# Optimization experiments

Measured on AMD Instinct MI355X. Metric: run time of the kernel, lower is better.

The kernel has to match this reference:

```python
import jax, jax.numpy as jnp
import numpy as np
import math

H = 8  # num_heads
# mock_theta_f Taylor coefficients: K(q) = 1 + q - 2q^2 + 3q^3
COEFFS = (1.0, 1.0, -2.0, 3.0)


def setup_inputs() -> dict:
    key = jax.random.key(0)
    ks = jax.random.split(key, 12)
    B, L, E = 2, 2048, 512
    s = 0.02
    return {
        "query": jax.random.normal(ks[0], (B, L, E), jnp.float32),
        "key_": jax.random.normal(ks[1], (B, L, E), jnp.float32),
        "value": jax.random.normal(ks[2], (B, L, E), jnp.float32),
        "Wq": jax.random.normal(ks[3], (E, E), jnp.float32) * s,
        "bq": jnp.zeros((E,), jnp.float32),
        "Wk": jax.random.normal(ks[4], (E, E), jnp.float32) * s,
        "bk": jnp.zeros((E,), jnp.float32),
        "Wv": jax.random.normal(ks[5], (E, E), jnp.float32) * s,
        "bv": jnp.zeros((E,), jnp.float32),
        "Wo": jax.random.normal(ks[6], (E, E), jnp.float32) * s,
        "bo": jnp.zeros((E,), jnp.float32),
        "log_tau": jnp.zeros((), jnp.float32),  # tau = exp(0) = 1.0
    }


def _horner(q):
    a0, a1, a2, a3 = COEFFS
    val = jnp.full_like(q, a3)
    val = q * val + a2
    val = q * val + a1
    val = q * val + a0
    return jnp.maximum(val, 0.0)


def _attn(query, key_, value, Wq, bq, Wk, bk, Wv, bv, Wo, bo, log_tau):
    B, L, E = query.shape
    S = key_.shape[1]
    Hd = E // H
    scale = math.sqrt(Hd)

    Q = (query @ Wq.T + bq).reshape(B, L, H, Hd).transpose(0, 2, 1, 3)  # (B,H,L,Hd)
    K = (key_ @ Wk.T + bk).reshape(B, S, H, Hd).transpose(0, 2, 1, 3)
    V = (value @ Wv.T + bv).reshape(B, S, H, Hd).transpose(0, 2, 1, 3)

    scores = jnp.einsum("bhld,bhsd->bhls", Q, K) / scale  # (B,H,L,S)

    tau = jnp.exp(log_tau)
    q = jax.nn.sigmoid(scores / tau)
    kv = _horner(q)

    # causal mask (is_causal=True): mask strict upper triangle
    causal = jnp.triu(jnp.ones((L, S), dtype=bool), k=1)  # (L,S)
    kv = jnp.where(causal[None, None], 0.0, kv)

    denom = jnp.sum(kv, axis=-1, keepdims=True)
    weights = kv / jnp.maximum(denom, 1e-12)

    out = jnp.einsum("bhls,bhsd->bhld", weights, V)  # (B,H,L,Hd)
    out = out.transpose(0, 2, 1, 3).reshape(B, L, E)
    return out @ Wo.T + bo


def reference(query, key_, value, Wq, bq, Wk, bk, Wv, bv, Wo, bo, log_tau):
    return _attn(query, key_, value, Wq, bq, Wk, bk, Wv, bv, Wo, bo, log_tau)
```

## Files before the change

### kernel.cpp

```cpp
#include <hip/hip_runtime.h>
#include <hip/hip_bf16.h>


typedef __attribute__((ext_vector_type(8))) __bf16 bf16x8;
typedef __attribute__((ext_vector_type(4))) __bf16 bf16x4;
typedef __attribute__((ext_vector_type(4))) float f32x4;
typedef __attribute__((ext_vector_type(4))) int i32x4;

#define NB 2
#define NL 2048
#define NE 512
#define NH 8
#define HD 64
#define NROW (NB * NL)
#define NJOB 144

__device__ __forceinline__ void gload16(const void* g, void* l) {
  __builtin_amdgcn_global_load_lds(
      (const __attribute__((address_space(1))) void*)g,
      (__attribute__((address_space(3))) void*)l, 16, 0, 0);
}

__global__ __launch_bounds__(256) void cvt_all(
    const float* __restrict__ q, const float* __restrict__ k,
    const float* __restrict__ v, const float* __restrict__ w0,
    const float* __restrict__ w1, const float* __restrict__ w2,
    const float* __restrict__ w3, __bf16* __restrict__ qo,
    __bf16* __restrict__ ko, __bf16* __restrict__ vo, __bf16* __restrict__ o0,
    __bf16* __restrict__ o1, __bf16* __restrict__ o2,
    __bf16* __restrict__ o3) {
  const int gid = blockIdx.x * 256 + threadIdx.x;
  const float* s;
  __bf16* d;
  int i;
  if (gid < 3 * (1 << 19)) {
    const int seg = gid >> 19;
    i = gid & ((1 << 19) - 1);
    s = seg == 0 ? q : (seg == 1 ? k : v);
    d = seg == 0 ? qo : (seg == 1 ? ko : vo);
  } else {
    const int wid = gid - 3 * (1 << 19);
    const int seg = wid >> 16;
    i = wid & 0xFFFF;
    s = seg == 0 ? w0 : (seg == 1 ? w1 : (seg == 2 ? w2 : w3));
    d = seg == 0 ? o0 : (seg == 1 ? o1 : (seg == 2 ? o2 : o3));
  }
  float4 x = ((const float4*)s)[i];
  bf16x4 o = {(__bf16)x.x, (__bf16)x.y, (__bf16)x.z, (__bf16)x.w};
  ((bf16x4*)d)[i] = o;
}

template <int MODE>
__device__ __forceinline__ void gemm_body(const __bf16* __restrict__ A,
                                          const __bf16* __restrict__ W,
                                          const float* __restrict__ bias,
                                          __bf16* __restrict__ outb,
                                          float* __restrict__ outf) {
  __shared__ __align__(16) __bf16 As[128 * 64];
  __shared__ __align__(16) __bf16 Ws[128 * 64];

  const int tid = threadIdx.x;
  const int lane = tid & 63, w = tid >> 6;
  const int lr = lane & 15, lg = lane >> 4;
  const int brow = blockIdx.y * 128, bcol = blockIdx.x * 128;
  const int wr = (w >> 1) * 64, wc = (w & 1) * 64;

  f32x4 zero4 = {0.f, 0.f, 0.f, 0.f};
  f32x4 acc[4][4];
#pragma unroll
  for (int i = 0; i < 4; ++i)
#pragma unroll
    for (int j = 0; j < 4; ++j) acc[i][j] = zero4;

  for (int k0 = 0; k0 < NE; k0 += 64) {
    __syncthreads();
#pragma unroll
    for (int q = 0; q < 4; ++q) {
      const int cidx = tid + q * 256;
      const int rr = cidx >> 3, cc = (cidx & 7) * 8;
      gload16(A + (size_t)(brow + rr) * NE + k0 + cc, As + cidx * 8);
      gload16(W + (size_t)(bcol + rr) * NE + k0 + cc, Ws + cidx * 8);
    }
    __syncthreads();

#pragma unroll
    for (int kk = 0; kk < 2; ++kk) {
      bf16x8 af[4], wf[4];
#pragma unroll
      for (int mi = 0; mi < 4; ++mi)
        af[mi] =
            *(const bf16x8*)(As + (wr + mi * 16 + lr) * 64 + kk * 32 + lg * 8);
#pragma unroll
      for (int ni = 0; ni < 4; ++ni)
        wf[ni] =
            *(const bf16x8*)(Ws + (wc + ni * 16 + lr) * 64 + kk * 32 + lg * 8);
#pragma unroll
      for (int mi = 0; mi < 4; ++mi)
#pragma unroll
        for (int ni = 0; ni < 4; ++ni)
          acc[mi][ni] = __builtin_amdgcn_mfma_f32_16x16x32_bf16(
              af[mi], wf[ni], acc[mi][ni], 0, 0, 0);
    }
  }

#pragma unroll
  for (int mi = 0; mi < 4; ++mi) {
#pragma unroll
    for (int ni = 0; ni < 4; ++ni) {
      const int col = bcol + wc + ni * 16 + lr;
      const float bv = bias[col];
#pragma unroll
      for (int r = 0; r < 4; ++r) {
        const int row = brow + wr + mi * 16 + lg * 4 + r;
        const float v = acc[mi][ni][r] + bv;
        if (MODE == 0) {
          const int b = row >> 11, l = row & (NL - 1);
          const int h = col >> 6, d = col & 63;
          outb[(((size_t)b * NH + h) * NL + l) * HD + d] = (__bf16)v;
        } else if (MODE == 2) {
          const int b = row >> 11, l = row & (NL - 1);
          const int h = col >> 6, d = col & 63;
          outb[(((size_t)b * NH + h) * HD + d) * NL + l] = (__bf16)v;
        } else {
          outf[(size_t)row * NE + col] = v;
        }
      }
    }
  }
}

__global__ __launch_bounds__(256) void qkv_gemm(
    const __bf16* __restrict__ A0, const __bf16* __restrict__ A1,
    const __bf16* __restrict__ A2, const __bf16* __restrict__ W0,
    const __bf16* __restrict__ W1, const __bf16* __restrict__ W2,
    const float* __restrict__ b0, const float* __restrict__ b1,
    const float* __restrict__ b2, __bf16* __restrict__ O0,
    __bf16* __restrict__ O1, __bf16* __restrict__ O2) {
  const int z = blockIdx.z;
  if (z == 2) {
    gemm_body<2>(A2, W2, b2, O2, nullptr);
  } else {
    const __bf16* A = z == 0 ? A0 : A1;
    const __bf16* W = z == 0 ? W0 : W1;
    const float* bias = z == 0 ? b0 : b1;
    __bf16* O = z == 0 ? O0 : O1;
    gemm_body<0>(A, W, bias, O, nullptr);
  }
}

__global__ __launch_bounds__(256) void out_gemm(const __bf16* __restrict__ A,
                                                const __bf16* __restrict__ W,
                                                const float* __restrict__ bias,
                                                float* __restrict__ outf) {
  gemm_body<1>(A, W, bias, nullptr, outf);
}

template <int SLOTTED>
__global__ __launch_bounds__(256) void attn_kernel(
    const __bf16* __restrict__ Qg, const __bf16* __restrict__ Kg,
    const __bf16* __restrict__ VTg, float* __restrict__ numg,
    float* __restrict__ deng, const float* __restrict__ log_tau) {
  __shared__ __align__(16) __bf16 Kt[64][72];
  __shared__ __align__(16) __bf16 Vt[64][72];

  const int j = blockIdx.x;
  int qb, c;
  if (j < 32) {
    c = 0; qb = j;
  } else if (j < 60) {
    c = 1; qb = j - 28;
  } else if (j < 84) {
    c = 2; qb = j - 52;
  } else if (j < 104) {
    c = 3; qb = j - 72;
  } else if (j < 120) {
    c = 4; qb = j - 88;
  } else if (j < 132) {
    c = 5; qb = j - 100;
  } else if (j < 140) {
    c = 6; qb = j - 108;
  } else {
    c = 7; qb = j - 112;
  }
  const int bh = blockIdx.y;
  const __bf16* Qh = Qg + (size_t)bh * NL * HD;
  const __bf16* Kh = Kg + (size_t)bh * NL * HD;
  const __bf16* Vth = VTg + (size_t)bh * HD * NL;

  const int tid = threadIdx.x;
  const int lane = tid & 63, w = tid >> 6;
  const int lr = lane & 15, lg = lane >> 4;
  const float ninv = -1.44269504f / (8.0f * __expf(log_tau[0]));

  const int q0 = qb * 64;
  const int qg = q0 + w * 16 + lr;
  bf16x8 qf[2];
  qf[0] = *(const bf16x8*)(Qh + (size_t)qg * HD + lg * 8);
  qf[1] = *(const bf16x8*)(Qh + (size_t)qg * HD + 32 + lg * 8);

  f32x4 zero4 = {0.f, 0.f, 0.f, 0.f};
  f32x4 o_acc[4];
#pragma unroll
  for (int n = 0; n < 4; ++n) o_acc[n] = zero4;
  float den_l = 0.f;

  const int t0 = c * 4;
  const int t1 = min(t0 + 4, qb + 1);

  const int kr0 = tid >> 3, kc0 = (tid & 7) * 8;

  bf16x8 kpa = *(const bf16x8*)(Kh + (size_t)(t0 * 64 + kr0) * HD + kc0);
  bf16x8 kpb = *(const bf16x8*)(Kh + (size_t)(t0 * 64 + kr0 + 32) * HD + kc0);
  bf16x8 vpa = *(const bf16x8*)(Vth + (size_t)kr0 * NL + t0 * 64 + kc0);
  bf16x8 vpb = *(const bf16x8*)(Vth + (size_t)(kr0 + 32) * NL + t0 * 64 + kc0);

  const int idxA = (((lane & 16) << 1) + lr) * 4;
  const bool hi = (lane & 32) != 0;

  for (int t = t0; t < t1; ++t) {
    const int kv0 = t * 64;
    __syncthreads();
    *(bf16x8*)&Kt[kr0][kc0] = kpa;
    *(bf16x8*)&Kt[kr0 + 32][kc0] = kpb;
    *(bf16x8*)&Vt[kr0][kc0] = vpa;
    *(bf16x8*)&Vt[kr0 + 32][kc0] = vpb;
    __syncthreads();

    if (t + 1 < t1) {
      const int kn = (t + 1) * 64;
      kpa = *(const bf16x8*)(Kh + (size_t)(kn + kr0) * HD + kc0);
      kpb = *(const bf16x8*)(Kh + (size_t)(kn + kr0 + 32) * HD + kc0);
      vpa = *(const bf16x8*)(Vth + (size_t)kr0 * NL + kn + kc0);
      vpb = *(const bf16x8*)(Vth + (size_t)(kr0 + 32) * NL + kn + kc0);
    }

    f32x4 sacc[4];
#pragma unroll
    for (int si = 0; si < 4; ++si) sacc[si] = zero4;
#pragma unroll
    for (int kk = 0; kk < 2; ++kk) {
#pragma unroll
      for (int si = 0; si < 4; ++si) {
        bf16x8 kf = *(const bf16x8*)&Kt[si * 16 + lr][kk * 32 + lg * 8];
        sacc[si] = __builtin_amdgcn_mfma_f32_16x16x32_bf16(kf, qf[kk],
                                                           sacc[si], 0, 0, 0);
      }
    }

    unsigned pk[4][2];
#pragma unroll
    for (int si = 0; si < 4; ++si) {
      const int sb = kv0 + si * 16 + lg * 4;
      unsigned kbv[4];
#pragma unroll
      for (int r = 0; r < 4; ++r) {
        const float e = __builtin_amdgcn_exp2f(sacc[si][r] * ninv);
        const float qs = __builtin_amdgcn_rcpf(1.0f + e);
        float kvv = fmaf(qs, fmaf(qs, fmaf(qs, 3.0f, -2.0f), 1.0f), 1.0f);
        if (sb + r > qg) kvv = 0.0f;
        const __bf16 kb = (__bf16)kvv;
        den_l += (float)kb;
        kbv[r] = (unsigned)__builtin_bit_cast(unsigned short, kb);
      }
      pk[si][0] = kbv[0] | (kbv[1] << 16);
      pk[si][1] = kbv[2] | (kbv[3] << 16);
    }

#pragma unroll
    for (int kk = 0; kk < 2; ++kk) {
      const int sl = kk * 2, sh = kk * 2 + 1;
      const int a0 = __builtin_amdgcn_ds_bpermute(idxA, (int)pk[sl][0]);
      const int a1 = __builtin_amdgcn_ds_bpermute(idxA, (int)pk[sl][1]);
      const int b0 = __builtin_amdgcn_ds_bpermute(idxA + 64, (int)pk[sl][0]);
      const int b1 = __builtin_amdgcn_ds_bpermute(idxA + 64, (int)pk[sl][1]);
      const int c0 = __builtin_amdgcn_ds_bpermute(idxA, (int)pk[sh][0]);
      const int c1 = __builtin_amdgcn_ds_bpermute(idxA, (int)pk[sh][1]);
      const int d0 = __builtin_amdgcn_ds_bpermute(idxA + 64, (int)pk[sh][0]);
      const int d1 = __builtin_amdgcn_ds_bpermute(idxA + 64, (int)pk[sh][1]);
      i32x4 pw = {hi ? c0 : a0, hi ? c1 : a1, hi ? d0 : b0, hi ? d1 : b1};
      bf16x8 pf = __builtin_bit_cast(bf16x8, pw);
#pragma unroll
      for (int n = 0; n < 4; ++n) {
        bf16x8 vf = *(const bf16x8*)&Vt[n * 16 + lr][kk * 32 + lg * 8];
        o_acc[n] = __builtin_amdgcn_mfma_f32_16x16x32_bf16(pf, vf, o_acc[n],
                                                           0, 0, 0);
      }
    }
  }

  den_l += __shfl_xor(den_l, 16, 64);
  den_l += __shfl_xor(den_l, 32, 64);

  if (SLOTTED) {
    float* nslot = numg + (((size_t)bh * NJOB + j) << 12);
    const int lrow = w * 16 + lg * 4;
    if (lg == 0) {
      float* dslot = deng + (((size_t)bh * NJOB + j) << 6);
      dslot[w * 16 + lr] = den_l;
    }
#pragma unroll
    for (int n = 0; n < 4; ++n) {
      const int col = n * 16 + lr;
#pragma unroll
      for (int r = 0; r < 4; ++r) nslot[(lrow + r) * 64 + col] = o_acc[n][r];
    }
  } else {
    const int orow = q0 + w * 16 + lg * 4;
    if (lg == 0) atomicAdd(&deng[(size_t)bh * NL + q0 + w * 16 + lr], den_l);
#pragma unroll
    for (int n = 0; n < 4; ++n) {
      const int col = n * 16 + lr;
#pragma unroll
      for (int r = 0; r < 4; ++r)
        atomicAdd(&numg[((size_t)bh * NL + orow + r) * HD + col], o_acc[n][r]);
    }
  }
}

__global__ __launch_bounds__(256) void combine_slotted(
    const float* __restrict__ numS, const float* __restrict__ denS,
    __bf16* __restrict__ AO) {
  const int gid = blockIdx.x * 256 + threadIdx.x;
  const int d4 = gid & 15;
  const int row = gid >> 4;
  const int bh = row >> 11, l = row & (NL - 1);
  const int b = bh >> 3, h = bh & 7;
  const int qb = l >> 6, lrow = l & 63;
  const int nc = (qb >> 2) + 1;

  f32x4 acc = {0.f, 0.f, 0.f, 0.f};
  float d = 0.f;
  for (int c = 0; c < nc; ++c) {
    const int jj = qb + 2 * c * (15 - c);
    const size_t sb = (size_t)bh * NJOB + jj;
    acc += *(const f32x4*)(numS + ((sb << 6) + lrow) * 64 + d4 * 4);
    d += denS[(sb << 6) + lrow];
  }
  const float idv = __builtin_amdgcn_rcpf(fmaxf(d, 1e-12f));
  bf16x4 o = {(__bf16)(acc[0] * idv), (__bf16)(acc[1] * idv),
              (__bf16)(acc[2] * idv), (__bf16)(acc[3] * idv)};
  *(bf16x4*)&AO[((size_t)b * NL + l) * NE + h * HD + d4 * 4] = o;
}

__global__ __launch_bounds__(256) void combine_kernel(
    const float* __restrict__ numg, const float* __restrict__ deng,
    __bf16* __restrict__ AO) {
  const int gid = blockIdx.x * 256 + threadIdx.x;
  const int d4 = gid & 15;
  const int row = gid >> 4;
  const int bh = row >> 11, l = row & (NL - 1);
  const int b = bh >> 3, h = bh & 7;
  f32x4 n4 = ((const f32x4*)numg)[gid];
  const float idv = __builtin_amdgcn_rcpf(fmaxf(deng[row], 1e-12f));
  bf16x4 o = {(__bf16)(n4[0] * idv), (__bf16)(n4[1] * idv),
              (__bf16)(n4[2] * idv), (__bf16)(n4[3] * idv)};
  *(bf16x4*)&AO[((size_t)b * NL + l) * NE + h * HD + d4 * 4] = o;
}

extern "C" void kernel_launch(void* const* d_in, const int* in_sizes, int n_in,
                              void* d_out, int out_size, void* d_ws,
                              size_t ws_size, hipStream_t stream) {
  const float* query = (const float*)d_in[0];
  const float* key_ = (const float*)d_in[1];
  const float* value = (const float*)d_in[2];
  const float* Wq = (const float*)d_in[3];
  const float* bq = (const float*)d_in[4];
  const float* Wk = (const float*)d_in[5];
  const float* bk = (const float*)d_in[6];
  const float* Wv = (const float*)d_in[7];
  const float* bv = (const float*)d_in[8];
  const float* Wo = (const float*)d_in[9];
  const float* bo = (const float*)d_in[10];
  const float* log_tau = (const float*)d_in[11];

  char* ws = (char*)d_ws;
  const size_t MB = 1024 * 1024;
  const bool slotted = (ws_size >= 55 * MB);

  __bf16* xb = (__bf16*)(ws + 0 * MB);
  __bf16* kxb = (__bf16*)(ws + 4 * MB);
  __bf16* vxb = (__bf16*)(ws + 8 * MB);

  __bf16 *wqb, *wkb, *wvb, *wob, *Qh, *Kh, *VT, *AO;
  float *numb, *denb;
  if (slotted) {
    numb = (float*)(ws + 0 * MB);
    denb = (float*)(ws + 36 * MB);
    wqb = (__bf16*)(ws + 37 * MB);
    wkb = (__bf16*)(ws + 37 * MB + 512 * 1024);
    wvb = (__bf16*)(ws + 38 * MB);
    wob = (__bf16*)(ws + 38 * MB + 512 * 1024);
    Qh = (__bf16*)(ws + 39 * MB);
    Kh = (__bf16*)(ws + 43 * MB);
    VT = (__bf16*)(ws + 47 * MB);
    AO = (__bf16*)(ws + 51 * MB);
  } else {
    numb = (float*)(ws + 0 * MB);
    denb = (float*)(ws + 8 * MB);
    wqb = (__bf16*)(ws + 12 * MB);
    wkb = (__bf16*)(ws + 12 * MB + 512 * 1024);
    wvb = (__bf16*)(ws + 13 * MB);
    wob = (__bf16*)(ws + 13 * MB + 512 * 1024);
    Qh = (__bf16*)(ws + 14 * MB);
    Kh = (__bf16*)(ws + 18 * MB);
    VT = (__bf16*)(ws + 22 * MB);
    AO = (__bf16*)(ws + 26 * MB);
  }

  cvt_all<<<7168, 256, 0, stream>>>(query, key_, value, Wq, Wk, Wv, Wo, xb,
                                    kxb, vxb, wqb, wkb, wvb, wob);

  dim3 gq(NE / 128, NROW / 128, 3);
  qkv_gemm<<<gq, 256, 0, stream>>>(xb, kxb, vxb, wqb, wkb, wvb, bq, bk, bv, Qh,
                                   Kh, VT);

  dim3 ga(NJOB, NB * NH);
  if (slotted) {
    attn_kernel<1><<<ga, 256, 0, stream>>>(Qh, Kh, VT, numb, denb, log_tau);
    combine_slotted<<<2048, 256, 0, stream>>>(numb, denb, AO);
  } else {
    hipMemsetAsync(ws, 0, 8 * MB + 128 * 1024, stream);
    attn_kernel<0><<<ga, 256, 0, stream>>>(Qh, Kh, VT, numb, denb, log_tau);
    combine_kernel<<<2048, 256, 0, stream>>>(numb, denb, AO);
  }

  dim3 gg(NE / 128, NROW / 128);
  out_gemm<<<gg, 256, 0, stream>>>(AO, wob, bo, (float*)d_out);
}
```

Measured before the change: 78.07 us.

## Fuse slotted combine into attention via last-block-arrives counter reduction

```diff
diff --git a/kernel.cpp b/kernel.cpp
--- a/kernel.cpp
+++ b/kernel.cpp
@@ -27,8 +27,12 @@
     const float* __restrict__ w1, const float* __restrict__ w2,
     const float* __restrict__ w3, __bf16* __restrict__ qo,
     __bf16* __restrict__ ko, __bf16* __restrict__ vo, __bf16* __restrict__ o0,
-    __bf16* __restrict__ o1, __bf16* __restrict__ o2,
-    __bf16* __restrict__ o3) {
+    __bf16* __restrict__ o1, __bf16* __restrict__ o2, __bf16* __restrict__ o3,
+    int* __restrict__ cnt) {
+  if (blockIdx.x == 7168) {
+    ((int2*)cnt)[threadIdx.x] = make_int2(0, 0);
+    return;
+  }
   const int gid = blockIdx.x * 256 + threadIdx.x;
   const float* s;
   __bf16* d;
@@ -159,9 +163,11 @@
 __global__ __launch_bounds__(256) void attn_kernel(
     const __bf16* __restrict__ Qg, const __bf16* __restrict__ Kg,
     const __bf16* __restrict__ VTg, float* __restrict__ numg,
-    float* __restrict__ deng, const float* __restrict__ log_tau) {
+    float* __restrict__ deng, __bf16* __restrict__ AO,
+    int* __restrict__ cnt, const float* __restrict__ log_tau) {
   __shared__ __align__(16) __bf16 Kt[64][72];
   __shared__ __align__(16) __bf16 Vt[64][72];
+  __shared__ int s_last;
 
   const int j = blockIdx.x;
   int qb, c;
@@ -293,7 +299,7 @@
 
   if (SLOTTED) {
     float* nslot = numg + (((size_t)bh * NJOB + j) << 12);
-    const int lrow = w * 16 + lg * 4;
+    const int lrow0 = w * 16 + lg * 4;
     if (lg == 0) {
       float* dslot = deng + (((size_t)bh * NJOB + j) << 6);
       dslot[w * 16 + lr] = den_l;
@@ -302,7 +308,36 @@
     for (int n = 0; n < 4; ++n) {
       const int col = n * 16 + lr;
 #pragma unroll
-      for (int r = 0; r < 4; ++r) nslot[(lrow + r) * 64 + col] = o_acc[n][r];
+      for (int r = 0; r < 4; ++r) nslot[(lrow0 + r) * 64 + col] = o_acc[n][r];
+    }
+
+    const int nc = (qb >> 2) + 1;
+    __syncthreads();
+    if (tid == 0) {
+      __threadfence();
+      const int old = atomicAdd(&cnt[bh * 32 + qb], 1);
+      s_last = (old == nc - 1) ? 1 : 0;
+    }
+    __syncthreads();
+    if (s_last) {
+      __threadfence();
+      const int b = bh >> 3, h = bh & 7;
+      for (int e = tid; e < 1024; e += 256) {
+        const int lrow = e >> 4, d4 = e & 15;
+        f32x4 acc = zero4;
+        float dsum = 0.f;
+        for (int cc2 = 0; cc2 < nc; ++cc2) {
+          const int jj = qb + 2 * cc2 * (15 - cc2);
+          const size_t sb = (size_t)bh * NJOB + jj;
+          acc += *(const f32x4*)(numg + ((sb << 6) + lrow) * 64 + d4 * 4);
+          dsum += deng[(sb << 6) + lrow];
+        }
+        const float idv = __builtin_amdgcn_rcpf(fmaxf(dsum, 1e-12f));
+        const int l = q0 + lrow;
+        bf16x4 o = {(__bf16)(acc[0] * idv), (__bf16)(acc[1] * idv),
+                    (__bf16)(acc[2] * idv), (__bf16)(acc[3] * idv)};
+        *(bf16x4*)&AO[((size_t)b * NL + l) * NE + h * HD + d4 * 4] = o;
+      }
     }
   } else {
     const int orow = q0 + w * 16 + lg * 4;
@@ -315,31 +350,6 @@
         atomicAdd(&numg[((size_t)bh * NL + orow + r) * HD + col], o_acc[n][r]);
     }
   }
-}
-
-__global__ __launch_bounds__(256) void combine_slotted(
-    const float* __restrict__ numS, const float* __restrict__ denS,
-    __bf16* __restrict__ AO) {
-  const int gid = blockIdx.x * 256 + threadIdx.x;
-  const int d4 = gid & 15;
-  const int row = gid >> 4;
-  const int bh = row >> 11, l = row & (NL - 1);
-  const int b = bh >> 3, h = bh & 7;
-  const int qb = l >> 6, lrow = l & 63;
-  const int nc = (qb >> 2) + 1;
-
-  f32x4 acc = {0.f, 0.f, 0.f, 0.f};
-  float d = 0.f;
-  for (int c = 0; c < nc; ++c) {
-    const int jj = qb + 2 * c * (15 - c);
-    const size_t sb = (size_t)bh * NJOB + jj;
-    acc += *(const f32x4*)(numS + ((sb << 6) + lrow) * 64 + d4 * 4);
-    d += denS[(sb << 6) + lrow];
-  }
-  const float idv = __builtin_amdgcn_rcpf(fmaxf(d, 1e-12f));
-  bf16x4 o = {(__bf16)(acc[0] * idv), (__bf16)(acc[1] * idv),
-              (__bf16)(acc[2] * idv), (__bf16)(acc[3] * idv)};
-  *(bf16x4*)&AO[((size_t)b * NL + l) * NE + h * HD + d4 * 4] = o;
 }
 
 __global__ __launch_bounds__(256) void combine_kernel(
@@ -383,9 +393,11 @@
 
   __bf16 *wqb, *wkb, *wvb, *wob, *Qh, *Kh, *VT, *AO;
   float *numb, *denb;
+  int* cnt;
   if (slotted) {
     numb = (float*)(ws + 0 * MB);
     denb = (float*)(ws + 36 * MB);
+    cnt = (int*)(ws + 36 * MB + 640 * 1024);
     wqb = (__bf16*)(ws + 37 * MB);
     wkb = (__bf16*)(ws + 37 * MB + 512 * 1024);
     wvb = (__bf16*)(ws + 38 * MB);
@@ -397,6 +409,7 @@
   } else {
     numb = (float*)(ws + 0 * MB);
     denb = (float*)(ws + 8 * MB);
+    cnt = (int*)(ws + 8 * MB + 256 * 1024);
     wqb = (__bf16*)(ws + 12 * MB);
     wkb = (__bf16*)(ws + 12 * MB + 512 * 1024);
     wvb = (__bf16*)(ws + 13 * MB);
@@ -407,8 +420,8 @@
     AO = (__bf16*)(ws + 26 * MB);
   }
 
-  cvt_all<<<7168, 256, 0, stream>>>(query, key_, value, Wq, Wk, Wv, Wo, xb,
-                                    kxb, vxb, wqb, wkb, wvb, wob);
+  cvt_all<<<7169, 256, 0, stream>>>(query, key_, value, Wq, Wk, Wv, Wo, xb,
+                                    kxb, vxb, wqb, wkb, wvb, wob, cnt);
 
   dim3 gq(NE / 128, NROW / 128, 3);
   qkv_gemm<<<gq, 256, 0, stream>>>(xb, kxb, vxb, wqb, wkb, wvb, bq, bk, bv, Qh,
@@ -416,11 +429,12 @@
 
   dim3 ga(NJOB, NB * NH);
   if (slotted) {
-    attn_kernel<1><<<ga, 256, 0, stream>>>(Qh, Kh, VT, numb, denb, log_tau);
-    combine_slotted<<<2048, 256, 0, stream>>>(numb, denb, AO);
-  } else {
-    hipMemsetAsync(ws, 0, 8 * MB + 128 * 1024, stream);
-    attn_kernel<0><<<ga, 256, 0, stream>>>(Qh, Kh, VT, numb, denb, log_tau);
+    attn_kernel<1><<<ga, 256, 0, stream>>>(Qh, Kh, VT, numb, denb, AO, cnt,
+                                           log_tau);
+  } else {
+    hipMemsetAsync(numb, 0, 8 * MB + 128 * 1024, stream);
+    attn_kernel<0><<<ga, 256, 0, stream>>>(Qh, Kh, VT, numb, denb, AO, cnt,
+                                           log_tau);
     combine_kernel<<<2048, 256, 0, stream>>>(numb, denb, AO);
   }
 
```

Measured after the change: 293.8 us. +276.4%, slower.
